# Kernel optimization log

Measured on AMD Instinct MI355X. Metric: run time of the kernel, lower is better.

## Reference

```python
import jax, jax.numpy as jnp
import numpy as np

NEG_SLOPE = 0.2  # GATConv default negative_slope


def gat_conv(x, row, col, W, b, a_src, a_dst, N):
    # GATConv, heads=1, flow='target_to_source': i=row (central), j=col (neighbor)
    h = x @ W                                                   # [N, C]
    e = jax.nn.leaky_relu((h @ a_src)[col] + (h @ a_dst)[row], NEG_SLOPE)  # [E]
    m = jax.ops.segment_max(e, row, num_segments=N)             # segment softmax over row
    w = jnp.exp(e - m[row])
    denom = jax.ops.segment_sum(w, row, num_segments=N)
    alpha = w / (denom[row] + 1e-16)
    out = jax.ops.segment_sum(alpha[:, None] * h[col], row, num_segments=N)
    return out + b


def lstm_scan(xs_t, Wih, Whh, bih, bhh):
    # xs_t: [L, N, C] -> hidden states [L, N, H]; PyTorch gate order i,f,g,o
    H = Whh.shape[1]
    Nn = xs_t.shape[1]
    bias = bih + bhh
    def step(carry, xt):
        h, c = carry
        g = xt @ Wih.T + h @ Whh.T + bias
        i, f, gg, o = jnp.split(g, 4, axis=-1)
        c = jax.nn.sigmoid(f) * c + jax.nn.sigmoid(i) * jnp.tanh(gg)
        h = jax.nn.sigmoid(o) * jnp.tanh(c)
        return (h, c), h
    init = (jnp.zeros((Nn, H), xs_t.dtype), jnp.zeros((Nn, H), xs_t.dtype))
    _, hs = jax.lax.scan(step, init, xs_t)
    return hs


def jk_lstm(xst, Wih_f, Whh_f, bih_f, bhh_f, Wih_b, Whh_b, bih_b, bhh_b, att_W, att_b):
    # xst: [L, N, C]; bidirectional LSTM over layer dim, attention-weighted sum
    hf = lstm_scan(xst, Wih_f, Whh_f, bih_f, bhh_f)
    hb = lstm_scan(xst[::-1], Wih_b, Whh_b, bih_b, bhh_b)[::-1]
    h = jnp.concatenate([hf, hb], axis=-1)                      # [L, N, 2H]
    score = jnp.einsum('lnh,h->ln', h, att_W) + att_b           # [L, N]
    alpha = jax.nn.softmax(score, axis=0)                       # softmax over layers
    return jnp.einsum('lnc,ln->nc', xst, alpha)                 # [N, C]


def setup_inputs() -> dict:
    key = jax.random.key(0)
    ks = list(jax.random.split(key, 32))
    N, E, C = 50000, 800000, 128
    L = 3
    H = (L * C) // 2  # 192; PyG JumpingKnowledge lstm hidden size
    s = 0.05
    d = {}
    d['x'] = jax.random.normal(ks[0], (N, 3), jnp.float32)
    d['edge_index'] = jax.random.randint(ks[1], (2, E), 0, N, jnp.int64)
    d['gat_W0'] = jax.random.normal(ks[2], (3, C)) * 0.3
    d['gat_b0'] = jnp.zeros((C,))
    d['gat_as0'] = jax.random.normal(ks[3], (C,)) * s
    d['gat_ad0'] = jax.random.normal(ks[4], (C,)) * s
    d['gat_W'] = jax.random.normal(ks[5], (L - 1, C, C)) * s
    d['gat_b'] = jnp.zeros((L - 1, C))
    d['gat_as'] = jax.random.normal(ks[6], (L - 1, C)) * s
    d['gat_ad'] = jax.random.normal(ks[7], (L - 1, C)) * s
    d['lstm_Wih_f'] = jax.random.normal(ks[8], (4 * H, C)) * s
    d['lstm_Whh_f'] = jax.random.normal(ks[9], (4 * H, H)) * s
    d['lstm_bih_f'] = jnp.zeros((4 * H,))
    d['lstm_bhh_f'] = jnp.zeros((4 * H,))
    d['lstm_Wih_b'] = jax.random.normal(ks[10], (4 * H, C)) * s
    d['lstm_Whh_b'] = jax.random.normal(ks[11], (4 * H, H)) * s
    d['lstm_bih_b'] = jnp.zeros((4 * H,))
    d['lstm_bhh_b'] = jnp.zeros((4 * H,))
    d['att_W'] = jax.random.normal(ks[12], (2 * H,)) * s
    d['att_b'] = jnp.zeros((1,))
    d['nW1'] = jax.random.normal(ks[13], (C, C)) * s
    d['nb1'] = jnp.zeros((C,))
    d['nW2'] = jax.random.normal(ks[14], (C, 2)) * s
    d['nb2'] = jnp.zeros((2,))
    d['eW1'] = jax.random.normal(ks[15], (2 * C, C)) * s
    d['eb1'] = jnp.zeros((C,))
    d['eW2'] = jax.random.normal(ks[16], (C, 2)) * s
    d['eb2'] = jnp.zeros((2,))
    return d


def reference(x, edge_index, gat_W0, gat_b0, gat_as0, gat_ad0, gat_W, gat_b, gat_as, gat_ad,
              lstm_Wih_f, lstm_Whh_f, lstm_bih_f, lstm_bhh_f,
              lstm_Wih_b, lstm_Whh_b, lstm_bih_b, lstm_bhh_b,
              att_W, att_b, nW1, nb1, nW2, nb2, eW1, eb1, eW2, eb2):
    N = x.shape[0]
    row, col = edge_index[0], edge_index[1]
    xs = []
    h = jax.nn.relu(gat_conv(x, row, col, gat_W0, gat_b0, gat_as0, gat_ad0, N))
    xs.append(h)
    for l in range(gat_W.shape[0]):  # fixed small layer count
        h = jax.nn.relu(gat_conv(h, row, col, gat_W[l], gat_b[l], gat_as[l], gat_ad[l], N))
        xs.append(h)
    xst = jnp.stack(xs, axis=0)  # [L, N, C]
    h = jk_lstm(xst, lstm_Wih_f, lstm_Whh_f, lstm_bih_f, lstm_bhh_f,
                lstm_Wih_b, lstm_Whh_b, lstm_bih_b, lstm_bhh_b, att_W, att_b)
    # node classifier (dropout is identity in eval)
    node_out = jax.nn.softmax(jax.nn.relu(h @ nW1 + nb1) @ nW2 + nb2, axis=1)
    # edge representation gather + concat, then edge classifier
    edge_rep = jnp.concatenate([h[row], h[col]], axis=1)  # [E, 2C]
    edge_out = jax.nn.softmax(jax.nn.relu(edge_rep @ eW1 + eb1) @ eW2 + eb2, axis=1)
    return node_out, edge_out
```

## Files before the change

kernel.cpp:

```cpp
#include <hip/hip_runtime.h>
#include <cstdint>
#include <cstddef>


#define NIN 28
#define MAXJOBS 20

struct InPtrs { const void* p[NIN]; int n[NIN]; };

struct ConvJobs {
    const void* src[MAXJOBS];
    float* dst[MAXJOBS];
    int n[MAXJOBS];
    int ai[MAXJOBS];
    int blk0[MAXJOBS + 1];
    int njobs;
};

typedef short s16x4 __attribute__((ext_vector_type(4)));
typedef short s16x8 __attribute__((ext_vector_type(8)));
typedef float f32x4 __attribute__((ext_vector_type(4)));
typedef unsigned short u16x8 __attribute__((ext_vector_type(8)));

__device__ __forceinline__ float bf2f(unsigned short v) {
    unsigned int u = ((unsigned int)v) << 16;
    return __uint_as_float(u);
}

__device__ __forceinline__ unsigned short f2bf(float x) {
    unsigned int u = __float_as_uint(x);
    unsigned int r = u + 0x7fffu + ((u >> 16) & 1u);
    return (unsigned short)(r >> 16);
}

__device__ __forceinline__ float rdx(const void* p, size_t i, int isf32) {
    return isf32 ? ((const float*)p)[i] : bf2f(((const unsigned short*)p)[i]);
}

__device__ __forceinline__ float frcp(float x) {
    return __builtin_amdgcn_rcpf(x);
}

__device__ __forceinline__ float sigm(float x) {
    return frcp(1.f + __expf(-x));
}

__device__ __forceinline__ float fast_tanh(float x) {
    return 1.f - 2.f * frcp(__expf(2.f * x) + 1.f);
}

__global__ void k_sniff(InPtrs in, int* flags) {
    int ai = blockIdx.x;
    if (ai >= NIN) return;
    __shared__ int cnt;
    if (threadIdx.x == 0) cnt = 0;
    __syncthreads();
    if (ai == 1) {
        const int* w = (const int*)in.p[1];
        int nw = in.n[1] < 512 ? in.n[1] : 512;
        int local = 0;
        for (int i = threadIdx.x; i < nw; i += blockDim.x)
            if ((i & 1) && w[i] != 0) local++;
        atomicAdd(&cnt, local);
        __syncthreads();
        if (threadIdx.x == 0) flags[1] = (cnt < 4) ? 1 : 0;
        return;
    }
    const unsigned short* u = (const unsigned short*)in.p[ai];
    int ns = in.n[ai] < 256 ? in.n[ai] : 256;
    int local = 0;
    for (int i = threadIdx.x; i < ns; i += blockDim.x) {
        if (i & 1) continue;
        unsigned short v = u[i];
        int e = (v >> 7) & 0xff;
        if ((v & 0x7fff) != 0 && (e < 100 || e > 154)) local++;
    }
    atomicAdd(&cnt, local);
    __syncthreads();
    if (threadIdx.x == 0) flags[ai] = (cnt * 4 >= ns) ? 1 : 0;
}

__global__ void k_convall(ConvJobs J, const int* __restrict__ flags) {
    int b = blockIdx.x;
    int j = 0;
    while (j + 1 < J.njobs && b >= J.blk0[j + 1]) ++j;
    int i = (b - J.blk0[j]) * 256 + threadIdx.x;
    if (i >= J.n[j]) return;
    J.dst[j][i] = rdx(J.src[j], i, flags[J.ai[j]]);
}

__global__ void k_conve(const void* src, int* row, int* col, int* cnt,
                        int E, const int* flags) {
    int i = blockIdx.x * blockDim.x + threadIdx.x;
    if (i >= E) return;
    int r, c;
    if (flags[1]) {
        const long long* s = (const long long*)src;
        r = (int)s[i];
        c = (int)s[(size_t)E + i];
    } else {
        const int* s = (const int*)src;
        r = s[i];
        c = s[(size_t)E + i];
    }
    row[i] = r;
    col[i] = c;
    atomicAdd(&cnt[r], 1);
}

__global__ void k_scan1(const int* __restrict__ deg, int* __restrict__ indptr,
                        int* __restrict__ bsums, int N) {
    __shared__ int buf[1024];
    const int t = threadIdx.x;
    const int base = blockIdx.x * 1024;
    int v = (base + t < N) ? deg[base + t] : 0;
    buf[t] = v;
    __syncthreads();
    for (int ofs = 1; ofs < 1024; ofs <<= 1) {
        int add = (t >= ofs) ? buf[t - ofs] : 0;
        __syncthreads();
        buf[t] += add;
        __syncthreads();
    }
    if (base + t < N) indptr[base + t] = buf[t] - v;
    if (t == 1023) bsums[blockIdx.x] = buf[1023];
}

__global__ void k_scan2(int* bsums, int nb) {
    if (threadIdx.x == 0 && blockIdx.x == 0) {
        int acc = 0;
        for (int j = 0; j < nb; ++j) { int v = bsums[j]; bsums[j] = acc; acc += v; }
        bsums[nb] = acc;
    }
}

__global__ void k_scan3(const int* __restrict__ bsums, int* __restrict__ indptr,
                        int* __restrict__ cnt, int N, int nb) {
    int i = blockIdx.x * blockDim.x + threadIdx.x;
    if (i < N) {
        indptr[i] += bsums[i >> 10];
        cnt[i] = 0;
    }
    if (i == 0) indptr[N] = bsums[nb];
}

__global__ void k_fill(const int* __restrict__ row, const int* __restrict__ col,
                       const int* __restrict__ indptr, int* __restrict__ cur,
                       int* __restrict__ colS, int* __restrict__ eidx, int E) {
    int i = blockIdx.x * blockDim.x + threadIdx.x;
    if (i >= E) return;
    int r = row[i];
    int p = indptr[r] + atomicAdd(&cur[r], 1);
    colS[p] = col[i];
    eidx[p] = i;
}

__global__ __launch_bounds__(256) void k_lin0(
    const float* __restrict__ x, const float* __restrict__ W0,
    const float* __restrict__ asrc, const float* __restrict__ adst,
    unsigned short* __restrict__ hlin, float* __restrict__ hs, float* __restrict__ hd,
    int N) {
    const int wid = threadIdx.x >> 6, lane = threadIdx.x & 63;
    const int n = blockIdx.x * 4 + wid;
    if (n >= N) return;
    float x0 = x[(size_t)n * 3], x1 = x[(size_t)n * 3 + 1], x2 = x[(size_t)n * 3 + 2];
    const int c0 = lane, c1 = lane + 64;
    float h0 = x0 * W0[c0] + x1 * W0[128 + c0] + x2 * W0[256 + c0];
    float h1 = x0 * W0[c1] + x1 * W0[128 + c1] + x2 * W0[256 + c1];
    hlin[(size_t)n * 128 + c0] = f2bf(h0);
    hlin[(size_t)n * 128 + c1] = f2bf(h1);
    float sp = h0 * asrc[c0] + h1 * asrc[c1];
    float dp = h0 * adst[c0] + h1 * adst[c1];
    for (int o = 32; o; o >>= 1) { sp += __shfl_down(sp, o); dp += __shfl_down(dp, o); }
    if (lane == 0) { hs[n] = sp; hd[n] = dp; }
}

__global__ __launch_bounds__(256) void k_lin(
    const unsigned short* __restrict__ xin, const float* __restrict__ W,
    const float* __restrict__ asrc, const float* __restrict__ adst,
    unsigned short* __restrict__ hlin, float* __restrict__ hs, float* __restrict__ hd,
    int N) {
    __shared__ float xl[16][128];
    const int t = threadIdx.x;
    const int wid = t >> 6, lane = t & 63;
    const int nb = blockIdx.x * 16;
    for (int i = t; i < 2048; i += 256) {
        int r = i >> 7, k = i & 127;
        int n = nb + r;
        xl[r][k] = (n < N) ? bf2f(xin[(size_t)n * 128 + k]) : 0.f;
    }
    __syncthreads();
    const int c0 = lane, c1 = lane + 64;
    const int r0 = wid * 4;
    float h0[4], h1[4];
    #pragma unroll
    for (int j = 0; j < 4; ++j) { h0[j] = 0.f; h1[j] = 0.f; }
    #pragma unroll 2
    for (int k = 0; k < 128; ++k) {
        float w0 = W[k * 128 + c0], w1 = W[k * 128 + c1];
        #pragma unroll
        for (int j = 0; j < 4; ++j) {
            float xv = xl[r0 + j][k];
            h0[j] += xv * w0;
            h1[j] += xv * w1;
        }
    }
    float sp[4], dp[4];
    #pragma unroll
    for (int j = 0; j < 4; ++j) {
        sp[j] = h0[j] * asrc[c0] + h1[j] * asrc[c1];
        dp[j] = h0[j] * adst[c0] + h1[j] * adst[c1];
    }
    #pragma unroll
    for (int o = 32; o; o >>= 1) {
        #pragma unroll
        for (int j = 0; j < 4; ++j) {
            sp[j] += __shfl_down(sp[j], o);
            dp[j] += __shfl_down(dp[j], o);
        }
    }
    #pragma unroll
    for (int j = 0; j < 4; ++j) {
        int n = nb + r0 + j;
        if (n < N) {
            hlin[(size_t)n * 128 + c0] = f2bf(h0[j]);
            hlin[(size_t)n * 128 + c1] = f2bf(h1[j]);
            if (lane == 0) { hs[n] = sp[j]; hd[n] = dp[j]; }
        }
    }
}

__global__ __launch_bounds__(256) void k_aggr(
    const unsigned short* __restrict__ hlin, const float* __restrict__ hs,
    const float* __restrict__ hd,
    const int* __restrict__ indptr, const int* __restrict__ colS,
    const float* __restrict__ b, unsigned short* __restrict__ xout, int N) {
    const int wid = threadIdx.x >> 6, lane = threadIdx.x & 63;
    const int n = blockIdx.x * 4 + wid;
    if (n >= N) return;
    const int s = indptr[n], epos = indptr[n + 1];
    const float hdv = hd[n];
    const int c0 = lane, c1 = lane + 64;
    float m = -1e30f, d = 0.f, a0 = 0.f, a1 = 0.f;
    int idx = s;
    for (; idx + 8 <= epos; idx += 8) {
        int cl[8];
        #pragma unroll
        for (int j = 0; j < 8; ++j) cl[j] = colS[idx + j];
        float e[8];
        #pragma unroll
        for (int j = 0; j < 8; ++j) {
            float ev = hs[cl[j]] + hdv;
            e[j] = (ev > 0.f) ? ev : 0.2f * ev;
        }
        float v0[8], v1[8];
        #pragma unroll
        for (int j = 0; j < 8; ++j) {
            const unsigned short* hp = hlin + (size_t)cl[j] * 128;
            v0[j] = bf2f(hp[c0]);
            v1[j] = bf2f(hp[c1]);
        }
        float m8 = e[0];
        #pragma unroll
        for (int j = 1; j < 8; ++j) m8 = fmaxf(m8, e[j]);
        if (m8 > m) {
            float sc = __expf(m - m8);
            a0 *= sc; a1 *= sc; d *= sc; m = m8;
        }
        #pragma unroll
        for (int j = 0; j < 8; ++j) {
            float w = __expf(e[j] - m);
            a0 += w * v0[j];
            a1 += w * v1[j];
            d  += w;
        }
    }
    for (; idx < epos; ++idx) {
        int col = colS[idx];
        float e = hs[col] + hdv;
        e = (e > 0.f) ? e : 0.2f * e;
        const unsigned short* hr = hlin + (size_t)col * 128;
        float v0 = bf2f(hr[c0]), v1 = bf2f(hr[c1]);
        if (e > m) {
            float sc = __expf(m - e);
            a0 = a0 * sc + v0;
            a1 = a1 * sc + v1;
            d  = d * sc + 1.f;
            m  = e;
        } else {
            float w = __expf(e - m);
            a0 += w * v0;
            a1 += w * v1;
            d  += w;
        }
    }
    float inv = frcp(d + 1e-16f);
    float r0 = a0 * inv + b[c0];
    float r1 = a1 * inv + b[c1];
    xout[(size_t)n * 128 + c0] = f2bf(fmaxf(r0, 0.f));
    xout[(size_t)n * 128 + c1] = f2bf(fmaxf(r1, 0.f));
}

__global__ void k_wpack(const void* Wihf, const void* Whhf,
                        const void* Wihb, const void* Whhb,
                        const void* bihf, const void* bhhf,
                        const void* bihb, const void* bhhb,
                        const int* __restrict__ flags,
                        unsigned short* __restrict__ Bpack, float* __restrict__ bsum) {
    int idx = blockIdx.x * blockDim.x + threadIdx.x;
    const int TOT = 2 * 10 * 48 * 512;
    if (idx < TOT) {
        int dir = idx / (10 * 48 * 512);
        int r   = idx % (10 * 48 * 512);
        int kb  = r / (48 * 512);
        int r2  = r % (48 * 512);
        int f   = r2 / 512;
        int q   = r2 % 512;
        int lane = q >> 3, j = q & 7;
        int k   = kb * 32 + ((j >> 2) * 16) + ((lane >> 4) * 4) + (j & 3);
        int col = f * 16 + (lane & 15);
        float v;
        if (k < 128)
            v = dir ? rdx(Wihb, (size_t)col * 128 + k, flags[14])
                    : rdx(Wihf, (size_t)col * 128 + k, flags[10]);
        else
            v = dir ? rdx(Whhb, (size_t)col * 192 + (k - 128), flags[15])
                    : rdx(Whhf, (size_t)col * 192 + (k - 128), flags[11]);
        Bpack[idx] = f2bf(v);
    }
    if (idx < 2 * 768) {
        int d = idx / 768, j = idx % 768;
        bsum[idx] = d ? rdx(bihb, j, flags[16]) + rdx(bhhb, j, flags[17])
                      : rdx(bihf, j, flags[12]) + rdx(bhhf, j, flags[13]);
    }
}

__global__ __launch_bounds__(768, 3) void k_lstm_mfma(
    const unsigned short* __restrict__ xsb,
    const unsigned short* __restrict__ Bpack,
    const float* __restrict__ bsum,
    const float* __restrict__ attW,
    float* __restrict__ scoreP,
    int N) {
    __shared__ unsigned short AS[64][332];
    __shared__ float scoreS[64];
    const int t = threadIdx.x;
    const int bf = t >> 6, lane = t & 63;
    const int dir = blockIdx.y;
    const int n0 = blockIdx.x * 64;
    const int ccol = lane & 15;
    const int klane = lane >> 4;
    const int lrow = klane * 4;
    const int akl = klane * 4;
    const int m = bf * 16 + ccol;

    const float bI = bsum[dir * 768 + m];
    const float bF = bsum[dir * 768 + 192 + m];
    const float bG = bsum[dir * 768 + 384 + m];
    const float bO = bsum[dir * 768 + 576 + m];
    const float awt = attW[dir * 192 + m];
    float cst[16];
    #pragma unroll
    for (int i = 0; i < 16; ++i) cst[i] = 0.f;

    const unsigned short* Bd = Bpack + (size_t)dir * 10 * 48 * 512;

    for (int s = 0; s < 3; ++s) {
        const int l = dir ? (2 - s) : s;
        {
            const unsigned short* xsrc = xsb + ((size_t)l * N + n0) * 128;
            for (int i = t; i < 1024; i += 768) {
                int r = i >> 4, kq = (i & 15) * 8;
                u16x8 v = (u16x8)(0);
                if (n0 + r < N) v = *(const u16x8*)(xsrc + (size_t)r * 128 + kq);
                *(u16x8*)&AS[r][kq] = v;
            }
        }
        if (t < 64) scoreS[t] = 0.f;
        __syncthreads();

        const int KB = s ? 10 : 4;
        f32x4 acc[4][4];
        #pragma unroll
        for (int rf = 0; rf < 4; ++rf)
            #pragma unroll
            for (int g = 0; g < 4; ++g) acc[rf][g] = (f32x4)(0.f);
        s16x8 bA[4], bB[4];
        {
            const unsigned short* bb = Bd + (size_t)bf * 512 + lane * 8;
            #pragma unroll
            for (int g = 0; g < 4; ++g) bA[g] = *(const s16x8*)(bb + (size_t)g * 6144);
        }
        for (int kb = 0; kb < KB; kb += 2) {
            {
                const unsigned short* bb = Bd + ((size_t)(kb + 1) * 48 + bf) * 512 + lane * 8;
                #pragma unroll
                for (int g = 0; g < 4; ++g) bB[g] = *(const s16x8*)(bb + (size_t)g * 6144);
            }
            {
                const int k0 = kb * 32 + akl;
                s16x8 av[4];
                #pragma unroll
                for (int rf = 0; rf < 4; ++rf) {
                    s16x4 alo = *(const s16x4*)&AS[rf * 16 + ccol][k0];
                    s16x4 ahi = *(const s16x4*)&AS[rf * 16 + ccol][k0 + 16];
                    av[rf] = __builtin_shufflevector(alo, ahi, 0, 1, 2, 3, 4, 5, 6, 7);
                }
                #pragma unroll
                for (int rf = 0; rf < 4; ++rf)
                    #pragma unroll
                    for (int g = 0; g < 4; ++g)
                        acc[rf][g] = __builtin_amdgcn_mfma_f32_16x16x32_bf16(
                            av[rf], bA[g], acc[rf][g], 0, 0, 0);
            }
            if (kb + 2 < KB) {
                const unsigned short* bb = Bd + ((size_t)(kb + 2) * 48 + bf) * 512 + lane * 8;
                #pragma unroll
                for (int g = 0; g < 4; ++g) bA[g] = *(const s16x8*)(bb + (size_t)g * 6144);
            }
            {
                const int k0 = (kb + 1) * 32 + akl;
                s16x8 av[4];
                #pragma unroll
                for (int rf = 0; rf < 4; ++rf) {
                    s16x4 alo = *(const s16x4*)&AS[rf * 16 + ccol][k0];
                    s16x4 ahi = *(const s16x4*)&AS[rf * 16 + ccol][k0 + 16];
                    av[rf] = __builtin_shufflevector(alo, ahi, 0, 1, 2, 3, 4, 5, 6, 7);
                }
                #pragma unroll
                for (int rf = 0; rf < 4; ++rf)
                    #pragma unroll
                    for (int g = 0; g < 4; ++g)
                        acc[rf][g] = __builtin_amdgcn_mfma_f32_16x16x32_bf16(
                            av[rf], bB[g], acc[rf][g], 0, 0, 0);
            }
        }
        __syncthreads();

        float sp[16];
        #pragma unroll
        for (int rf = 0; rf < 4; ++rf) {
            #pragma unroll
            for (int reg = 0; reg < 4; ++reg) {
                float gI = acc[rf][0][reg] + bI;
                float gF = acc[rf][1][reg] + bF;
                float gG = acc[rf][2][reg] + bG;
                float gO = acc[rf][3][reg] + bO;
                float ig = sigm(gI);
                float fg = sigm(gF);
                float gt = fast_tanh(gG);
                float og = sigm(gO);
                int ci = rf * 4 + reg;
                float cn = fg * cst[ci] + ig * gt;
                cst[ci] = cn;
                float hh = og * fast_tanh(cn);
                AS[rf * 16 + lrow + reg][128 + m] = f2bf(hh);
                sp[ci] = hh * awt;
            }
        }
        #pragma unroll
        for (int o = 1; o < 16; o <<= 1) {
            #pragma unroll
            for (int i = 0; i < 16; ++i) sp[i] += __shfl_xor(sp[i], o);
        }
        if (ccol == 0) {
            #pragma unroll
            for (int i = 0; i < 16; ++i)
                atomicAdd(&scoreS[(i >> 2) * 16 + lrow + (i & 3)], sp[i]);
        }
        __syncthreads();
        if (t < 64 && n0 + t < N)
            scoreP[(size_t)(dir * 3 + l) * N + n0 + t] = scoreS[t];
    }
}

__global__ __launch_bounds__(256) void k_tail(
    const unsigned short* __restrict__ xsb, const float* __restrict__ scoreP,
    const float* __restrict__ nW1, const float* __restrict__ nb1,
    const float* __restrict__ nW2, const float* __restrict__ nb2,
    const float* __restrict__ eW1, const float* __restrict__ eb1,
    unsigned short* __restrict__ P, unsigned short* __restrict__ Q,
    float* __restrict__ out, int N) {
    __shared__ float xl[16][128];
    __shared__ float al[16][4];
    const int t = threadIdx.x;
    const int wid = t >> 6, lane = t & 63;
    const int nb = blockIdx.x * 16;
    if (t < 16) {
        int n = nb + t;
        float e0 = 0.f, e1 = 0.f, e2 = 0.f;
        if (n < N) {
            float s0 = scoreP[n]                 + scoreP[(size_t)3 * N + n];
            float s1 = scoreP[(size_t)N + n]     + scoreP[(size_t)4 * N + n];
            float s2 = scoreP[(size_t)2 * N + n] + scoreP[(size_t)5 * N + n];
            float mm = fmaxf(s0, fmaxf(s1, s2));
            e0 = __expf(s0 - mm); e1 = __expf(s1 - mm); e2 = __expf(s2 - mm);
            float inv = frcp(e0 + e1 + e2);
            e0 *= inv; e1 *= inv; e2 *= inv;
        }
        al[t][0] = e0; al[t][1] = e1; al[t][2] = e2;
    }
    __syncthreads();
    const size_t L1o = (size_t)N * 128, L2o = 2 * L1o;
    for (int i = t; i < 2048; i += 256) {
        int r = i >> 7, k = i & 127;
        int n = nb + r;
        float v = 0.f;
        if (n < N) {
            size_t p = (size_t)n * 128 + k;
            v = al[r][0] * bf2f(xsb[p]) + al[r][1] * bf2f(xsb[L1o + p])
              + al[r][2] * bf2f(xsb[L2o + p]);
        }
        xl[r][k] = v;
    }
    __syncthreads();
    const int c0 = lane, c1 = lane + 64;
    const int r0 = wid * 4;
    {
        float h0[4], h1[4];
        #pragma unroll
        for (int j = 0; j < 4; ++j) { h0[j] = 0.f; h1[j] = 0.f; }
        #pragma unroll 2
        for (int k = 0; k < 128; ++k) {
            float w0 = nW1[k * 128 + c0], w1 = nW1[k * 128 + c1];
            #pragma unroll
            for (int j = 0; j < 4; ++j) {
                float xv = xl[r0 + j][k];
                h0[j] += xv * w0;
                h1[j] += xv * w1;
            }
        }
        float p0[4], p1[4];
        #pragma unroll
        for (int j = 0; j < 4; ++j) {
            float a = fmaxf(h0[j] + nb1[c0], 0.f);
            float bq = fmaxf(h1[j] + nb1[c1], 0.f);
            p0[j] = a * nW2[c0 * 2 + 0] + bq * nW2[c1 * 2 + 0];
            p1[j] = a * nW2[c0 * 2 + 1] + bq * nW2[c1 * 2 + 1];
        }
        #pragma unroll
        for (int o = 32; o; o >>= 1) {
            #pragma unroll
            for (int j = 0; j < 4; ++j) {
                p0[j] += __shfl_down(p0[j], o);
                p1[j] += __shfl_down(p1[j], o);
            }
        }
        if (lane == 0) {
            #pragma unroll
            for (int j = 0; j < 4; ++j) {
                int n = nb + r0 + j;
                if (n < N) {
                    float l0 = p0[j] + nb2[0], l1 = p1[j] + nb2[1];
                    float mm = fmaxf(l0, l1);
                    float e0 = __expf(l0 - mm), e1 = __expf(l1 - mm);
                    float inv = frcp(e0 + e1);
                    out[2 * (size_t)n]     = e0 * inv;
                    out[2 * (size_t)n + 1] = e1 * inv;
                }
            }
        }
    }
    {
        float pp0[4], pp1[4], qq0[4], qq1[4];
        #pragma unroll
        for (int j = 0; j < 4; ++j) { pp0[j] = 0.f; pp1[j] = 0.f; qq0[j] = 0.f; qq1[j] = 0.f; }
        for (int k = 0; k < 128; ++k) {
            float wp0 = eW1[k * 128 + c0], wp1 = eW1[k * 128 + c1];
            float wq0 = eW1[(128 + k) * 128 + c0], wq1 = eW1[(128 + k) * 128 + c1];
            #pragma unroll
            for (int j = 0; j < 4; ++j) {
                float xv = xl[r0 + j][k];
                pp0[j] += xv * wp0; pp1[j] += xv * wp1;
                qq0[j] += xv * wq0; qq1[j] += xv * wq1;
            }
        }
        #pragma unroll
        for (int j = 0; j < 4; ++j) {
            int n = nb + r0 + j;
            if (n < N) {
                P[(size_t)n * 128 + c0] = f2bf(pp0[j] + eb1[c0]);
                P[(size_t)n * 128 + c1] = f2bf(pp1[j] + eb1[c1]);
                Q[(size_t)n * 128 + c0] = f2bf(qq0[j]);
                Q[(size_t)n * 128 + c1] = f2bf(qq1[j]);
            }
        }
    }
}

__global__ __launch_bounds__(256) void k_edge3(
    const unsigned short* __restrict__ P, const unsigned short* __restrict__ Q,
    const int* __restrict__ indptr, const int* __restrict__ colS,
    const int* __restrict__ eidx,
    const float* __restrict__ W2, const float* __restrict__ b2,
    float* __restrict__ out, int N) {
    const int wid = threadIdx.x >> 6, lane = threadIdx.x & 63;
    const int n = blockIdx.x * 4 + wid;
    if (n >= N) return;
    const int sl = lane & 15, g = lane >> 4;
    const int s = indptr[n], e = indptr[n + 1];
    float pf[8];
    {
        u16x8 pv = *(const u16x8*)(P + (size_t)n * 128 + sl * 8);
        #pragma unroll
        for (int j = 0; j < 8; ++j) pf[j] = bf2f(pv[j]);
    }
    const float* W2f = W2;
    const float b20 = b2[0], b21 = b2[1];
    for (int p = s + g; p < e; p += 8) {
        int p1 = p + 4;
        bool v1 = p1 < e;
        int col0 = colS[p],  eo0 = eidx[p];
        int col1 = v1 ? colS[p1] : col0;
        int eo1  = v1 ? eidx[p1] : 0;
        u16x8 qv0 = *(const u16x8*)(Q + (size_t)col0 * 128 + sl * 8);
        u16x8 qv1 = *(const u16x8*)(Q + (size_t)col1 * 128 + sl * 8);
        float l00 = 0.f, l01 = 0.f, l10 = 0.f, l11 = 0.f;
        #pragma unroll
        for (int j = 0; j < 8; ++j) {
            int ch = sl * 8 + j;
            float wA = W2f[ch * 2], wB = W2f[ch * 2 + 1];
            float h0 = fmaxf(pf[j] + bf2f(qv0[j]), 0.f);
            float h1 = fmaxf(pf[j] + bf2f(qv1[j]), 0.f);
            l00 += h0 * wA; l01 += h0 * wB;
            l10 += h1 * wA; l11 += h1 * wB;
        }
        #pragma unroll
        for (int o = 1; o < 16; o <<= 1) {
            l00 += __shfl_xor(l00, o); l01 += __shfl_xor(l01, o);
            l10 += __shfl_xor(l10, o); l11 += __shfl_xor(l11, o);
        }
        if (sl == 0) {
            {
                float a = l00 + b20, b = l01 + b21;
                float mm = fmaxf(a, b);
                float e0 = __expf(a - mm), e1 = __expf(b - mm);
                float inv = frcp(e0 + e1);
                out[2 * (size_t)N + 2 * (size_t)eo0]     = e0 * inv;
                out[2 * (size_t)N + 2 * (size_t)eo0 + 1] = e1 * inv;
            }
            if (v1) {
                float a = l10 + b20, b = l11 + b21;
                float mm = fmaxf(a, b);
                float e0 = __expf(a - mm), e1 = __expf(b - mm);
                float inv = frcp(e0 + e1);
                out[2 * (size_t)N + 2 * (size_t)eo1]     = e0 * inv;
                out[2 * (size_t)N + 2 * (size_t)eo1 + 1] = e1 * inv;
            }
        }
    }
}

extern "C" void kernel_launch(void* const* d_in, const int* in_sizes, int n_in,
                              void* d_out, int out_size, void* d_ws, size_t ws_size,
                              hipStream_t stream) {
    if (n_in < NIN) return;
    const int N = in_sizes[0] / 3;
    const int E = in_sizes[1] / 2;

    char* ws = (char*)d_ws;
    size_t off = 0;
    auto alloc = [&](size_t bytes) -> char* {
        char* p = ws + off;
        off = (off + bytes + 255) & ~(size_t)255;
        return p;
    };
    int* flags = (int*)alloc(32 * sizeof(int));
    int* bsums = (int*)alloc(128 * sizeof(int));
    float* canon[NIN];
    for (int i = 0; i < NIN; ++i) canon[i] = nullptr;
    for (int i = 0; i < NIN; ++i) {
        if (i == 1 || (i >= 10 && i <= 17)) continue;
        canon[i] = (float*)alloc((size_t)in_sizes[i] * 4);
    }
    int* row32  = (int*)alloc((size_t)E * 4);
    int* col32  = (int*)alloc((size_t)E * 4);
    int* indptr = (int*)alloc((size_t)(N + 1) * 4);
    int* cnt    = (int*)alloc((size_t)N * 4);
    int* colS   = (int*)alloc((size_t)E * 4);
    int* eidx   = (int*)alloc((size_t)E * 4);
    float* hs   = (float*)alloc((size_t)N * 4);
    float* hd   = (float*)alloc((size_t)N * 4);
    float* hJK  = (float*)alloc((size_t)N * 128 * 4);
    unsigned short* hlin = (unsigned short*)hJK;
    unsigned short* xsb = (unsigned short*)alloc((size_t)3 * N * 128 * 2);
    unsigned short* Bpack = (unsigned short*)alloc((size_t)2 * 10 * 48 * 512 * 2);
    float* bsum = (float*)alloc((size_t)2 * 768 * 4);
    float* scoreP = (float*)alloc((size_t)6 * N * 4);
    if (off > ws_size) return;
    unsigned short* P = (unsigned short*)hJK;
    unsigned short* Q = (unsigned short*)hJK + (size_t)N * 128;

    InPtrs ip;
    for (int i = 0; i < NIN; ++i) { ip.p[i] = d_in[i]; ip.n[i] = in_sizes[i]; }

    k_sniff<<<NIN, 256, 0, stream>>>(ip, flags);

    {
        ConvJobs J;
        int nj = 0, blk = 0;
        for (int i = 0; i < NIN; ++i) {
            if (i == 1 || (i >= 10 && i <= 17)) continue;
            J.src[nj] = d_in[i];
            J.dst[nj] = canon[i];
            J.n[nj] = in_sizes[i];
            J.ai[nj] = i;
            J.blk0[nj] = blk;
            blk += (in_sizes[i] + 255) / 256;
            ++nj;
        }
        J.blk0[nj] = blk;
        J.njobs = nj;
        k_convall<<<blk, 256, 0, stream>>>(J, flags);
    }
    hipMemsetAsync(cnt, 0, (size_t)N * 4, stream);
    k_conve<<<(E + 255) / 256, 256, 0, stream>>>(d_in[1], row32, col32, cnt, E, flags);
    k_wpack<<<(2 * 10 * 48 * 512 + 255) / 256, 256, 0, stream>>>(
        d_in[10], d_in[11], d_in[14], d_in[15],
        d_in[12], d_in[13], d_in[16], d_in[17], flags, Bpack, bsum);

    const int nb1k = (N + 1023) / 1024;
    k_scan1<<<nb1k, 1024, 0, stream>>>(cnt, indptr, bsums, N);
    k_scan2<<<1, 64, 0, stream>>>(bsums, nb1k);
    k_scan3<<<(N + 255) / 256, 256, 0, stream>>>(bsums, indptr, cnt, N, nb1k);
    k_fill<<<(E + 255) / 256, 256, 0, stream>>>(row32, col32, indptr, cnt, colS, eidx, E);

    k_lin0<<<(N + 3) / 4, 256, 0, stream>>>(canon[0], canon[2], canon[4], canon[5],
                                            hlin, hs, hd, N);
    k_aggr<<<(N + 3) / 4, 256, 0, stream>>>(hlin, hs, hd, indptr, colS, canon[3], xsb, N);
    for (int l = 1; l < 3; ++l) {
        const float* W  = canon[6] + (size_t)(l - 1) * 128 * 128;
        const float* bb = canon[7] + (size_t)(l - 1) * 128;
        const float* as = canon[8] + (size_t)(l - 1) * 128;
        const float* ad = canon[9] + (size_t)(l - 1) * 128;
        k_lin<<<(N + 15) / 16, 256, 0, stream>>>(xsb + (size_t)(l - 1) * N * 128, W, as, ad,
                                                 hlin, hs, hd, N);
        k_aggr<<<(N + 3) / 4, 256, 0, stream>>>(hlin, hs, hd, indptr, colS, bb,
                                                xsb + (size_t)l * N * 128, N);
    }

    dim3 lgrid((N + 63) / 64, 2);
    k_lstm_mfma<<<lgrid, 768, 0, stream>>>(xsb, Bpack, bsum, canon[18], scoreP, N);

    float* out = (float*)d_out;
    k_tail<<<(N + 15) / 16, 256, 0, stream>>>(xsb, scoreP,
                                              canon[20], canon[21], canon[22], canon[23],
                                              canon[24], canon[25], P, Q, out, N);
    k_edge3<<<(N + 3) / 4, 256, 0, stream>>>(P, Q, indptr, colS, eidx,
                                             canon[26], canon[27], out, N);
}
```

Baseline: 703.6 us.

## Replace scalar GAT linear layer with bf16 MFMA kernel and prepacked weights

```diff
diff --git a/kernel.cpp b/kernel.cpp
--- a/kernel.cpp
+++ b/kernel.cpp
@@ -175,59 +175,100 @@
     if (lane == 0) { hs[n] = sp; hd[n] = dp; }
 }
 
-__global__ __launch_bounds__(256) void k_lin(
-    const unsigned short* __restrict__ xin, const float* __restrict__ W,
+__global__ void k_wpackg(const float* __restrict__ Wcanon,
+                         unsigned short* __restrict__ Wg) {
+    int idx = blockIdx.x * blockDim.x + threadIdx.x;
+    if (idx >= 2 * 4 * 8 * 512) return;
+    int layer = idx / 16384;
+    int r  = idx % 16384;
+    int kb = r / 4096;
+    int r2 = r % 4096;
+    int f  = r2 / 512;
+    int q  = r2 % 512;
+    int lane = q >> 3, j = q & 7;
+    int k   = kb * 32 + ((j >> 2) * 16) + ((lane >> 4) * 4) + (j & 3);
+    int col = f * 16 + (lane & 15);
+    Wg[idx] = f2bf(Wcanon[(size_t)layer * 16384 + (size_t)k * 128 + col]);
+}
+
+__global__ __launch_bounds__(512) void k_linm(
+    const unsigned short* __restrict__ xin,
+    const unsigned short* __restrict__ Wg,
     const float* __restrict__ asrc, const float* __restrict__ adst,
     unsigned short* __restrict__ hlin, float* __restrict__ hs, float* __restrict__ hd,
     int N) {
-    __shared__ float xl[16][128];
+    __shared__ unsigned short AS[64][136];
+    __shared__ float hsS[64], hdS[64];
     const int t = threadIdx.x;
-    const int wid = t >> 6, lane = t & 63;
-    const int nb = blockIdx.x * 16;
-    for (int i = t; i < 2048; i += 256) {
-        int r = i >> 7, k = i & 127;
-        int n = nb + r;
-        xl[r][k] = (n < N) ? bf2f(xin[(size_t)n * 128 + k]) : 0.f;
-    }
+    const int f = t >> 6, lane = t & 63;
+    const int n0 = blockIdx.x * 64;
+    const int ccol = lane & 15;
+    const int klane = lane >> 4;
+    const int lrow = klane * 4;
+    const int akl = klane * 4;
+    const int m = f * 16 + ccol;
+
+    const float asv = asrc[m], adv = adst[m];
+
+    for (int i = t; i < 1024; i += 512) {
+        int r = i >> 4, kq = (i & 15) * 8;
+        u16x8 v = (u16x8)(0);
+        if (n0 + r < N) v = *(const u16x8*)(xin + (size_t)(n0 + r) * 128 + kq);
+        *(u16x8*)&AS[r][kq] = v;
+    }
+    if (t < 64) { hsS[t] = 0.f; hdS[t] = 0.f; }
     __syncthreads();
-    const int c0 = lane, c1 = lane + 64;
-    const int r0 = wid * 4;
-    float h0[4], h1[4];
+
+    f32x4 acc[4];
     #pragma unroll
-    for (int j = 0; j < 4; ++j) { h0[j] = 0.f; h1[j] = 0.f; }
-    #pragma unroll 2
-    for (int k = 0; k < 128; ++k) {
-        float w0 = W[k * 128 + c0], w1 = W[k * 128 + c1];
-        #pragma unroll
-        for (int j = 0; j < 4; ++j) {
-            float xv = xl[r0 + j][k];
-            h0[j] += xv * w0;
-            h1[j] += xv * w1;
-        }
-    }
-    float sp[4], dp[4];
+    for (int rf = 0; rf < 4; ++rf) acc[rf] = (f32x4)(0.f);
     #pragma unroll
-    for (int j = 0; j < 4; ++j) {
-        sp[j] = h0[j] * asrc[c0] + h1[j] * asrc[c1];
-        dp[j] = h0[j] * adst[c0] + h1[j] * adst[c1];
-    }
+    for (int kb = 0; kb < 4; ++kb) {
+        s16x8 b = *(const s16x8*)(Wg + ((size_t)kb * 8 + f) * 512 + lane * 8);
+        const int k0 = kb * 32 + akl;
+        #pragma unroll
+        for (int rf = 0; rf < 4; ++rf) {
+            s16x4 alo = *(const s16x4*)&AS[rf * 16 + ccol][k0];
+            s16x4 ahi = *(const s16x4*)&AS[rf * 16 + ccol][k0 + 16];
+            s16x8 av = __builtin_shufflevector(alo, ahi, 0, 1, 2, 3, 4, 5, 6, 7);
+            acc[rf] = __builtin_amdgcn_mfma_f32_16x16x32_bf16(av, b, acc[rf], 0, 0, 0);
+        }
+    }
+    __syncthreads();
+
+    float sp[16], dp[16];
     #pragma unroll
-    for (int o = 32; o; o >>= 1) {
-        #pragma unroll
-        for (int j = 0; j < 4; ++j) {
-            sp[j] += __shfl_down(sp[j], o);
-            dp[j] += __shfl_down(dp[j], o);
+    for (int rf = 0; rf < 4; ++rf) {
+        #pragma unroll
+        for (int reg = 0; reg < 4; ++reg) {
+            float h = acc[rf][reg];
+            int ci = rf * 4 + reg;
+            AS[rf * 16 + lrow + reg][m] = f2bf(h);
+            sp[ci] = h * asv;
+            dp[ci] = h * adv;
         }
     }
     #pragma unroll
-    for (int j = 0; j < 4; ++j) {
-        int n = nb + r0 + j;
-        if (n < N) {
-            hlin[(size_t)n * 128 + c0] = f2bf(h0[j]);
-            hlin[(size_t)n * 128 + c1] = f2bf(h1[j]);
-            if (lane == 0) { hs[n] = sp[j]; hd[n] = dp[j]; }
-        }
-    }
+    for (int o = 1; o < 16; o <<= 1) {
+        #pragma unroll
+        for (int i = 0; i < 16; ++i) { sp[i] += __shfl_xor(sp[i], o); dp[i] += __shfl_xor(dp[i], o); }
+    }
+    if (ccol == 0) {
+        #pragma unroll
+        for (int i = 0; i < 16; ++i) {
+            int row = (i >> 2) * 16 + lrow + (i & 3);
+            atomicAdd(&hsS[row], sp[i]);
+            atomicAdd(&hdS[row], dp[i]);
+        }
+    }
+    __syncthreads();
+
+    for (int i = t; i < 1024; i += 512) {
+        int r = i >> 4, kq = (i & 15) * 8;
+        if (n0 + r < N)
+            *(u16x8*)(hlin + (size_t)(n0 + r) * 128 + kq) = *(const u16x8*)&AS[r][kq];
+    }
+    if (t < 64 && n0 + t < N) { hs[n0 + t] = hsS[t]; hd[n0 + t] = hdS[t]; }
 }
 
 __global__ __launch_bounds__(256) void k_aggr(
@@ -685,6 +726,7 @@
     unsigned short* hlin = (unsigned short*)hJK;
     unsigned short* xsb = (unsigned short*)alloc((size_t)3 * N * 128 * 2);
     unsigned short* Bpack = (unsigned short*)alloc((size_t)2 * 10 * 48 * 512 * 2);
+    unsigned short* Wg = (unsigned short*)alloc((size_t)2 * 4 * 8 * 512 * 2);
     float* bsum = (float*)alloc((size_t)2 * 768 * 4);
     float* scoreP = (float*)alloc((size_t)6 * N * 4);
     if (off > ws_size) return;
@@ -718,6 +760,7 @@
     k_wpack<<<(2 * 10 * 48 * 512 + 255) / 256, 256, 0, stream>>>(
         d_in[10], d_in[11], d_in[14], d_in[15],
         d_in[12], d_in[13], d_in[16], d_in[17], flags, Bpack, bsum);
+    k_wpackg<<<(2 * 4 * 8 * 512 + 255) / 256, 256, 0, stream>>>(canon[6], Wg);
 
     const int nb1k = (N + 1023) / 1024;
     k_scan1<<<nb1k, 1024, 0, stream>>>(cnt, indptr, bsums, N);
@@ -729,12 +772,12 @@
                                             hlin, hs, hd, N);
     k_aggr<<<(N + 3) / 4, 256, 0, stream>>>(hlin, hs, hd, indptr, colS, canon[3], xsb, N);
     for (int l = 1; l < 3; ++l) {
-        const float* W  = canon[6] + (size_t)(l - 1) * 128 * 128;
+        const unsigned short* Wgl = Wg + (size_t)(l - 1) * 4 * 8 * 512;
         const float* bb = canon[7] + (size_t)(l - 1) * 128;
         const float* as = canon[8] + (size_t)(l - 1) * 128;
         const float* ad = canon[9] + (size_t)(l - 1) * 128;
-        k_lin<<<(N + 15) / 16, 256, 0, stream>>>(xsb + (size_t)(l - 1) * N * 128, W, as, ad,
-                                                 hlin, hs, hd, N);
+        k_linm<<<(N + 63) / 64, 512, 0, stream>>>(xsb + (size_t)(l - 1) * N * 128, Wgl,
+                                                  as, ad, hlin, hs, hd, N);
         k_aggr<<<(N + 3) / 4, 256, 0, stream>>>(hlin, hs, hd, indptr, colS, bb,
                                                 xsb + (size_t)l * N * 128, N);
     }
```

Result: faster. 671.7 us (-4.5%).
